# Kernel optimization log

Hardware: AMD Instinct MI355X
Metric: run time of the kernel (lower is better)

Reference implementation:

```python
import jax, jax.numpy as jnp
import numpy as np

B, C, W, H = 4, 512, 64, 64
CK = C // 8  # channels // k


def setup_inputs() -> dict:
    key = jax.random.key(0)
    ks = jax.random.split(key, 10)
    s = 0.02
    return {
        "x": jax.random.normal(ks[0], (B, C, W, H), jnp.float32),
        "wf": jax.random.normal(ks[1], (CK, C), jnp.float32) * s,
        "bf": jax.random.normal(ks[2], (CK,), jnp.float32) * s,
        "wg": jax.random.normal(ks[3], (CK, C), jnp.float32) * s,
        "bg": jax.random.normal(ks[4], (CK,), jnp.float32) * s,
        "wh": jax.random.normal(ks[5], (CK, C), jnp.float32) * s,
        "bh": jax.random.normal(ks[6], (CK,), jnp.float32) * s,
        "wv": jax.random.normal(ks[7], (C, CK), jnp.float32) * s,
        "bv": jax.random.normal(ks[8], (C,), jnp.float32) * s,
        "gamma": jax.random.normal(ks[9], (1,), jnp.float32) * 0.1,
    }


def reference(x, wf, bf, wg, bg, wh, bh, wv, bv, gamma):
    b, c, w, h = x.shape
    n = w * h  # location_num
    xf = x.reshape(b, c, n)  # (B, C, N)
    # conv1x1 projections == per-location matmuls
    f = jnp.einsum('oc,bcn->bon', wf, xf) + bf[None, :, None]  # (B, CK, N)
    g = jnp.einsum('oc,bcn->bon', wg, xf) + bg[None, :, None]
    hh = jnp.einsum('oc,bcn->bon', wh, xf) + bh[None, :, None]
    # beta[b, i, j] = sum_c f[b,c,i] * g[b,c,j]; softmax over dim=1 (i axis)
    beta = jax.nn.softmax(jnp.einsum('bcn,bcm->bnm', f, g), axis=1)  # (B, N, N)
    h2 = jnp.einsum('bcn,bnm->bcm', hh, beta)  # (B, CK, N)
    o = jnp.einsum('oc,bcn->bon', wv, h2) + bv[None, :, None]  # (B, C, N)
    y = gamma[0] * o + xf
    return y.reshape(b, c, w, h)
```

## Files before the change

### kernel.cpp

```cpp
#include <hip/hip_runtime.h>
#include <stdint.h>

#define B_ 4
#define C_ 512
#define N_ 4096
#define D_ 64
#define LOG2E 1.4426950408889634f

typedef __attribute__((ext_vector_type(8))) short short8;
typedef __attribute__((ext_vector_type(4))) float f32x4;
typedef __attribute__((ext_vector_type(16))) float f32x16;
typedef unsigned short ushort_t;

static __device__ __forceinline__ ushort_t f2bf(float f) {
    union { float f; uint32_t u; } v; v.f = f;
    uint32_t u = v.u;
    uint32_t r = u + 0x7FFFu + ((u >> 16) & 1u);
    return (ushort_t)(r >> 16);
}
static __device__ __forceinline__ float bf2f(uint32_t u) {
    union { uint32_t u; float f; } v; v.u = u << 16;
    return v.f;
}
static __device__ __forceinline__ uint32_t cvtpk_bf16(float lo, float hi) {
    uint32_t r;
    asm("v_cvt_pk_bf16_f32 %0, %1, %2" : "=v"(r) : "v"(lo), "v"(hi));
    return r;
}
static __device__ __forceinline__ void gl16(const ushort_t* g, ushort_t* l) {
    __builtin_amdgcn_global_load_lds(
        (const __attribute__((address_space(1))) void*)g,
        (__attribute__((address_space(3))) void*)l, 16, 0, 0);
}

__global__ __launch_bounds__(512) void proj_fgh(
    const float* __restrict__ x,
    const float* __restrict__ wf, const float* __restrict__ bf,
    const float* __restrict__ wg, const float* __restrict__ bg,
    const float* __restrict__ wh, const float* __restrict__ bh,
    ushort_t* __restrict__ Ftf, ushort_t* __restrict__ Gt,
    ushort_t* __restrict__ Vtf)
{
    const int b    = blockIdx.y;
    const int tile = blockIdx.x;
    const int n0   = tile * 64;
    const int tid  = threadIdx.x;
    const int wv   = tid >> 6;
    const int mw   = wv & 3;
    const int hi   = wv >> 2;
    const int lane = tid & 63;
    const int g    = lane >> 4;
    const int r    = lane & 15;

    __shared__ ushort_t As[64][40];
    __shared__ ushort_t Bs[192][40];

    f32x4 acc[6];
    #pragma unroll
    for (int t = 0; t < 6; ++t) acc[t] = (f32x4){0.f, 0.f, 0.f, 0.f};

    const int ka = tid >> 4;
    const int mb = (tid & 15) * 4;
    const int kb = (tid & 7) * 4;
    const int ow = tid >> 3;

    const float* xp  = x  + ((size_t)b * C_ + ka) * N_ + n0 + mb;
    const float* wp0 = wf + (size_t)ow * C_ + kb;
    const float* wp1 = wg + (size_t)ow * C_ + kb;
    const float* wp2 = wh + (size_t)ow * C_ + kb;

    float4 xa = *(const float4*)xp;
    float4 w0 = *(const float4*)wp0;
    float4 w1 = *(const float4*)wp1;
    float4 w2 = *(const float4*)wp2;

    for (int k0 = 0; k0 < C_; k0 += 32) {
        As[mb + 0][ka] = f2bf(xa.x);
        As[mb + 1][ka] = f2bf(xa.y);
        As[mb + 2][ka] = f2bf(xa.z);
        As[mb + 3][ka] = f2bf(xa.w);
        {
            uint2 p0, p1, p2;
            p0.x = cvtpk_bf16(w0.x, w0.y); p0.y = cvtpk_bf16(w0.z, w0.w);
            p1.x = cvtpk_bf16(w1.x, w1.y); p1.y = cvtpk_bf16(w1.z, w1.w);
            p2.x = cvtpk_bf16(w2.x, w2.y); p2.y = cvtpk_bf16(w2.z, w2.w);
            *(uint2*)&Bs[ow][kb]       = p0;
            *(uint2*)&Bs[64 + ow][kb]  = p1;
            *(uint2*)&Bs[128 + ow][kb] = p2;
        }
        if (k0 + 32 < C_) {
            xa = *(const float4*)(xp + (size_t)(k0 + 32) * N_);
            w0 = *(const float4*)(wp0 + k0 + 32);
            w1 = *(const float4*)(wp1 + k0 + 32);
            w2 = *(const float4*)(wp2 + k0 + 32);
        }
        __syncthreads();
        short8 a = *(const short8*)&As[16 * mw + r][8 * g];
        __builtin_amdgcn_s_setprio(1);
        #pragma unroll
        for (int tt = 0; tt < 6; ++tt) {
            const int T = hi * 6 + tt;
            short8 bbv = *(const short8*)&Bs[T * 16 + r][8 * g];
            acc[tt] = __builtin_amdgcn_mfma_f32_16x16x32_bf16(a, bbv, acc[tt], 0, 0, 0);
        }
        __builtin_amdgcn_s_setprio(0);
        __syncthreads();
    }

    #pragma unroll
    for (int u = 0; u < 2; ++u) {
        const int tt = hi ? u : (4 + u);
        const int og = hi ? (32 + u * 16 + r) : (u * 16 + r);
        const float bvv = bg[og];
        #pragma unroll
        for (int j = 0; j < 4; ++j) {
            const int loc = n0 + 16 * mw + 4 * g + j;
            Gt[((size_t)b * N_ + loc) * D_ + og] = f2bf(acc[tt][j] + bvv);
        }
    }

    ushort_t (*bb)[72] = (ushort_t(*)[72])Bs;

    if (hi == 0) {
        #pragma unroll
        for (int tt = 0; tt < 4; ++tt) {
            const int o = tt * 16 + r;
            const float bvv = bf[o];
            #pragma unroll
            for (int j = 0; j < 4; ++j)
                bb[16 * mw + 4 * g + j][o] = f2bf((acc[tt][j] + bvv) * LOG2E);
        }
    }
    __syncthreads();
    {
        const int f  = wv;
        const int cc = f >> 2, s = f & 3;
        short8 v = *(const short8*)&bb[32 * cc + (lane & 31)][16 * s + 8 * (lane >> 5)];
        *(short8*)&Ftf[(((size_t)b * 64 + tile) * 8 + f) * 512 + lane * 8] = v;
    }
    __syncthreads();

    if (hi == 1) {
        #pragma unroll
        for (int tt = 2; tt < 6; ++tt) {
            const int o = (tt - 2) * 16 + r;
            const float bvv = bh[o];
            #pragma unroll
            for (int j = 0; j < 4; ++j)
                bb[16 * mw + 4 * g + j][o] = f2bf(acc[tt][j] + bvv);
        }
    }
    __syncthreads();
    {
        const int f   = wv;
        const int cc  = f >> 2, sub = (f >> 1) & 1, dt = f & 1;
        const int h2l = lane >> 5;
        short8 v;
        #pragma unroll
        for (int e = 0; e < 8; ++e) {
            const int i = 32 * cc + 16 * sub + (e & 3) + 8 * (e >> 2) + 4 * h2l;
            v[e] = (short)bb[i][32 * dt + (lane & 31)];
        }
        *(short8*)&Vtf[(((size_t)b * 64 + tile) * 8 + f) * 512 + lane * 8] = v;
    }
}

__global__ __launch_bounds__(256, 4) void attn(
    const ushort_t* __restrict__ Ftf, const ushort_t* __restrict__ Gt,
    const ushort_t* __restrict__ Vtf,
    ushort_t* __restrict__ Op, float* __restrict__ ml, int ksplit)
{
    const int b    = blockIdx.z;
    const int part = blockIdx.y;
    const int tid  = threadIdx.x;
    const int lane = tid & 63;
    const int wave = tid >> 6;
    const int l31  = lane & 31;
    const int h2   = lane >> 5;
    const int j0   = blockIdx.x * 128 + wave * 32;
    const int NT   = (N_ / ksplit) / 64;
    const int kt0  = part * NT;

    __shared__ __align__(16) ushort_t Ks[2][4096];
    __shared__ __align__(16) ushort_t Vs[2][4096];

    const ushort_t* qrow = Gt + ((size_t)b * N_ + j0 + l31) * D_ + 8 * h2;
    const short8 qf0 = *(const short8*)(qrow);
    const short8 qf1 = *(const short8*)(qrow + 16);
    const short8 qf2 = *(const short8*)(qrow + 32);
    const short8 qf3 = *(const short8*)(qrow + 48);

    const ushort_t* Kt = Ftf + ((size_t)b * 64 + kt0) * 4096;
    const ushort_t* Vt = Vtf + ((size_t)b * 64 + kt0) * 4096;

    f32x16 oA, oB;
    #pragma unroll
    for (int q = 0; q < 16; ++q) { oA[q] = 0.f; oB[q] = 0.f; }
    float l_run = 0.f;

    gl16(Kt + tid * 8,         &Ks[0][tid * 8]);
    gl16(Kt + (tid + 256) * 8, &Ks[0][(tid + 256) * 8]);
    gl16(Vt + tid * 8,         &Vs[0][tid * 8]);
    gl16(Vt + (tid + 256) * 8, &Vs[0][(tid + 256) * 8]);

    int buf = 0;
    for (int t = 0; t < NT; ++t) {
        __syncthreads();
        if (t + 1 < NT) {
            const ushort_t* kg = Kt + (size_t)(t + 1) * 4096;
            const ushort_t* vg = Vt + (size_t)(t + 1) * 4096;
            const int nb = buf ^ 1;
            gl16(kg + tid * 8,         &Ks[nb][tid * 8]);
            gl16(kg + (tid + 256) * 8, &Ks[nb][(tid + 256) * 8]);
            gl16(vg + tid * 8,         &Vs[nb][tid * 8]);
            gl16(vg + (tid + 256) * 8, &Vs[nb][(tid + 256) * 8]);
        }
        #pragma unroll
        for (int cc = 0; cc < 2; ++cc) {
            const ushort_t* kb0 = &Ks[buf][cc * 2048];
            f32x16 sx;
            #pragma unroll
            for (int q = 0; q < 16; ++q) sx[q] = 0.f;
            __builtin_amdgcn_s_setprio(1);
            {
                const short8 k0 = *(const short8*)(kb0 + 0 * 512 + lane * 8);
                sx = __builtin_amdgcn_mfma_f32_32x32x16_bf16(k0, qf0, sx, 0, 0, 0);
                const short8 k1 = *(const short8*)(kb0 + 1 * 512 + lane * 8);
                sx = __builtin_amdgcn_mfma_f32_32x32x16_bf16(k1, qf1, sx, 0, 0, 0);
                const short8 k2 = *(const short8*)(kb0 + 2 * 512 + lane * 8);
                sx = __builtin_amdgcn_mfma_f32_32x32x16_bf16(k2, qf2, sx, 0, 0, 0);
                const short8 k3 = *(const short8*)(kb0 + 3 * 512 + lane * 8);
                sx = __builtin_amdgcn_mfma_f32_32x32x16_bf16(k3, qf3, sx, 0, 0, 0);
            }
            __builtin_amdgcn_s_setprio(0);

            uint32_t pw[8];
            float cs = 0.f;
            #pragma unroll
            for (int q = 0; q < 8; ++q) {
                const float pa = __builtin_amdgcn_exp2f(sx[2 * q]);
                const float pb = __builtin_amdgcn_exp2f(sx[2 * q + 1]);
                cs += pa + pb;
                pw[q] = cvtpk_bf16(pa, pb);
            }
            l_run += cs;

            union { uint32_t w[4]; short8 v; } p0u, p1u;
            p0u.w[0] = pw[0]; p0u.w[1] = pw[1]; p0u.w[2] = pw[2]; p0u.w[3] = pw[3];
            p1u.w[0] = pw[4]; p1u.w[1] = pw[5]; p1u.w[2] = pw[6]; p1u.w[3] = pw[7];

            const ushort_t* vb0 = &Vs[buf][cc * 2048];
            __builtin_amdgcn_s_setprio(1);
            {
                const short8 v00 = *(const short8*)(vb0 + 0 * 512 + lane * 8);
                oA = __builtin_amdgcn_mfma_f32_32x32x16_bf16(v00, p0u.v, oA, 0, 0, 0);
                const short8 v01 = *(const short8*)(vb0 + 1 * 512 + lane * 8);
                oB = __builtin_amdgcn_mfma_f32_32x32x16_bf16(v01, p0u.v, oB, 0, 0, 0);
                const short8 v10 = *(const short8*)(vb0 + 2 * 512 + lane * 8);
                oA = __builtin_amdgcn_mfma_f32_32x32x16_bf16(v10, p1u.v, oA, 0, 0, 0);
                const short8 v11 = *(const short8*)(vb0 + 3 * 512 + lane * 8);
                oB = __builtin_amdgcn_mfma_f32_32x32x16_bf16(v11, p1u.v, oB, 0, 0, 0);
            }
            __builtin_amdgcn_s_setprio(0);
        }
        buf ^= 1;
    }

    const float lt = l_run + __shfl_xor(l_run, 32);

    ushort_t* orow = Op + (((size_t)b * ksplit + part) * N_ + j0 + l31) * D_;
    #pragma unroll
    for (int q = 0; q < 4; ++q) {
        const int d0 = 8 * q + 4 * h2;
        uint2 ua, ub;
        ua.x = cvtpk_bf16(oA[4 * q],     oA[4 * q + 1]);
        ua.y = cvtpk_bf16(oA[4 * q + 2], oA[4 * q + 3]);
        *(uint2*)&orow[d0] = ua;
        ub.x = cvtpk_bf16(oB[4 * q],     oB[4 * q + 1]);
        ub.y = cvtpk_bf16(oB[4 * q + 2], oB[4 * q + 3]);
        *(uint2*)&orow[32 + d0] = ub;
    }
    if (h2 == 0)
        ml[((size_t)b * ksplit + part) * N_ + j0 + l31] = lt;
}

__global__ __launch_bounds__(512) void reduce_outproj(
    const ushort_t* __restrict__ Op, const float* __restrict__ ml,
    const float* __restrict__ wv, const float* __restrict__ bv,
    const float* __restrict__ gamma, const float* __restrict__ x,
    float* __restrict__ y, int ksplit)
{
    const int b    = blockIdx.y;
    const int n0   = blockIdx.x * 64;
    const int tid  = threadIdx.x;
    const int wv8  = tid >> 6;
    const int lane = tid & 63;
    const int g    = lane >> 4;
    const int r    = lane & 15;

    __shared__ ushort_t Os[64][72];

    {
        const int loc = tid >> 3;
        const int k8  = (tid & 7) * 8;
        float L = 0.f;
        float v[8] = {0.f, 0.f, 0.f, 0.f, 0.f, 0.f, 0.f, 0.f};
        for (int p = 0; p < ksplit; ++p) {
            const size_t base = ((size_t)b * ksplit + p) * N_ + n0 + loc;
            L += ml[base];
            uint4 u = *(const uint4*)&Op[base * D_ + k8];
            v[0] += bf2f(u.x & 0xffffu); v[1] += bf2f(u.x >> 16);
            v[2] += bf2f(u.y & 0xffffu); v[3] += bf2f(u.y >> 16);
            v[4] += bf2f(u.z & 0xffffu); v[5] += bf2f(u.z >> 16);
            v[6] += bf2f(u.w & 0xffffu); v[7] += bf2f(u.w >> 16);
        }
        const float inv = 1.0f / L;
        uint4 o;
        o.x = cvtpk_bf16(v[0] * inv, v[1] * inv);
        o.y = cvtpk_bf16(v[2] * inv, v[3] * inv);
        o.z = cvtpk_bf16(v[4] * inv, v[5] * inv);
        o.w = cvtpk_bf16(v[6] * inv, v[7] * inv);
        *(uint4*)&Os[loc][k8] = o;
    }
    __syncthreads();

    short8 a[4][2];
    #pragma unroll
    for (int cs = 0; cs < 4; ++cs) {
        const float* wrow = wv + (size_t)(wv8 * 64 + cs * 16 + r) * D_ + 8 * g;
        const float4 wa = *(const float4*)(wrow);
        const float4 wb = *(const float4*)(wrow + 4);
        const float4 wc = *(const float4*)(wrow + 32);
        const float4 wd = *(const float4*)(wrow + 36);
        uint32_t* a0 = (uint32_t*)&a[cs][0];
        uint32_t* a1 = (uint32_t*)&a[cs][1];
        a0[0] = cvtpk_bf16(wa.x, wa.y); a0[1] = cvtpk_bf16(wa.z, wa.w);
        a0[2] = cvtpk_bf16(wb.x, wb.y); a0[3] = cvtpk_bf16(wb.z, wb.w);
        a1[0] = cvtpk_bf16(wc.x, wc.y); a1[1] = cvtpk_bf16(wc.z, wc.w);
        a1[2] = cvtpk_bf16(wd.x, wd.y); a1[3] = cvtpk_bf16(wd.z, wd.w);
    }

    f32x4 acc[4][4];
    #pragma unroll
    for (int cs = 0; cs < 4; ++cs)
        #pragma unroll
        for (int t = 0; t < 4; ++t) acc[cs][t] = (f32x4){0.f, 0.f, 0.f, 0.f};

    #pragma unroll
    for (int t = 0; t < 4; ++t) {
        const short8 b0 = *(const short8*)&Os[16 * t + r][8 * g];
        const short8 b1 = *(const short8*)&Os[16 * t + r][32 + 8 * g];
        __builtin_amdgcn_s_setprio(1);
        #pragma unroll
        for (int cs = 0; cs < 4; ++cs) {
            acc[cs][t] = __builtin_amdgcn_mfma_f32_16x16x32_bf16(a[cs][0], b0, acc[cs][t], 0, 0, 0);
            acc[cs][t] = __builtin_amdgcn_mfma_f32_16x16x32_bf16(a[cs][1], b1, acc[cs][t], 0, 0, 0);
        }
        __builtin_amdgcn_s_setprio(0);
    }

    const float gm = *gamma;
    #pragma unroll
    for (int cs = 0; cs < 4; ++cs) {
        #pragma unroll
        for (int t = 0; t < 4; ++t) {
            #pragma unroll
            for (int j = 0; j < 4; ++j) {
                const int co = wv8 * 64 + cs * 16 + 4 * g + j;
                const int n  = n0 + 16 * t + r;
                const size_t idx = ((size_t)b * C_ + co) * N_ + n;
                y[idx] = gm * (acc[cs][t][j] + bv[co]) + x[idx];
            }
        }
    }
}

extern "C" void kernel_launch(void* const* d_in, const int* in_sizes, int n_in,
                              void* d_out, int out_size, void* d_ws, size_t ws_size,
                              hipStream_t stream) {
    const float* x     = (const float*)d_in[0];
    const float* wf    = (const float*)d_in[1];
    const float* bf    = (const float*)d_in[2];
    const float* wg    = (const float*)d_in[3];
    const float* bg    = (const float*)d_in[4];
    const float* wh    = (const float*)d_in[5];
    const float* bh    = (const float*)d_in[6];
    const float* wv    = (const float*)d_in[7];
    const float* bv    = (const float*)d_in[8];
    const float* gamma = (const float*)d_in[9];
    float* y = (float*)d_out;

    const size_t plane = (size_t)B_ * N_ * D_;
    ushort_t* Ftf = (ushort_t*)d_ws;
    ushort_t* Gt  = Ftf + plane;
    ushort_t* Vtf = Gt + plane;
    ushort_t* Op  = Vtf + plane;

    int KS = 8;
    while (KS > 1) {
        const size_t need = 3 * plane * 2 + (size_t)KS * plane * 2
                          + (size_t)B_ * KS * N_ * sizeof(float);
        if (need <= ws_size) break;
        KS >>= 1;
    }
    float* ml = (float*)(Op + (size_t)KS * plane);

    proj_fgh<<<dim3(N_ / 64, B_), 512, 0, stream>>>(
        x, wf, bf, wg, bg, wh, bh, Ftf, Gt, Vtf);
    attn<<<dim3(N_ / 128, KS, B_), 256, 0, stream>>>(
        Ftf, Gt, Vtf, Op, ml, KS);
    reduce_outproj<<<dim3(N_ / 64, B_), 512, 0, stream>>>(
        Op, ml, wv, bv, gamma, x, y, KS);
}
```

Measured before the change: 60.11 us.

## Halve projection tile to 32 locations to double block count

The projection kernel now processes 32 spatial locations per block instead of 64, launching twice as many blocks so more CUs are occupied. Each wave computes 3 MFMA tiles (one each for F, G, H) instead of 6, and the epilogue writes F and H into separate shared-memory regions with a single barrier, splitting the Ftf/Vtf stores between the two thread halves. The weight tiles are still loaded and converted per block, so weight traffic and conversion work double relative to the x data.

```diff
diff --git a/kernel.cpp b/kernel.cpp
--- a/kernel.cpp
+++ b/kernel.cpp
@@ -42,34 +42,36 @@
     ushort_t* __restrict__ Vtf)
 {
     const int b    = blockIdx.y;
-    const int tile = blockIdx.x;
-    const int n0   = tile * 64;
+    const int nb   = blockIdx.x;
+    const int tile = nb >> 1;
+    const int cc   = nb & 1;
+    const int n0   = nb * 32;
     const int tid  = threadIdx.x;
     const int wv   = tid >> 6;
-    const int mw   = wv & 3;
-    const int hi   = wv >> 2;
+    const int mw   = wv & 1;
+    const int hi   = wv >> 1;
     const int lane = tid & 63;
     const int g    = lane >> 4;
     const int r    = lane & 15;
 
-    __shared__ ushort_t As[64][40];
+    __shared__ ushort_t As[32][40];
     __shared__ ushort_t Bs[192][40];
 
-    f32x4 acc[6];
-    #pragma unroll
-    for (int t = 0; t < 6; ++t) acc[t] = (f32x4){0.f, 0.f, 0.f, 0.f};
+    f32x4 acc[3];
+    #pragma unroll
+    for (int t = 0; t < 3; ++t) acc[t] = (f32x4){0.f, 0.f, 0.f, 0.f};
 
     const int ka = tid >> 4;
-    const int mb = (tid & 15) * 4;
+    const int mb = (tid & 15) * 2;
+    const int ow = tid >> 3;
     const int kb = (tid & 7) * 4;
-    const int ow = tid >> 3;
 
     const float* xp  = x  + ((size_t)b * C_ + ka) * N_ + n0 + mb;
     const float* wp0 = wf + (size_t)ow * C_ + kb;
     const float* wp1 = wg + (size_t)ow * C_ + kb;
     const float* wp2 = wh + (size_t)ow * C_ + kb;
 
-    float4 xa = *(const float4*)xp;
+    float2 xa = *(const float2*)xp;
     float4 w0 = *(const float4*)wp0;
     float4 w1 = *(const float4*)wp1;
     float4 w2 = *(const float4*)wp2;
@@ -77,8 +79,6 @@
     for (int k0 = 0; k0 < C_; k0 += 32) {
         As[mb + 0][ka] = f2bf(xa.x);
         As[mb + 1][ka] = f2bf(xa.y);
-        As[mb + 2][ka] = f2bf(xa.z);
-        As[mb + 3][ka] = f2bf(xa.w);
         {
             uint2 p0, p1, p2;
             p0.x = cvtpk_bf16(w0.x, w0.y); p0.y = cvtpk_bf16(w0.z, w0.w);
@@ -89,7 +89,7 @@
             *(uint2*)&Bs[128 + ow][kb] = p2;
         }
         if (k0 + 32 < C_) {
-            xa = *(const float4*)(xp + (size_t)(k0 + 32) * N_);
+            xa = *(const float2*)(xp + (size_t)(k0 + 32) * N_);
             w0 = *(const float4*)(wp0 + k0 + 32);
             w1 = *(const float4*)(wp1 + k0 + 32);
             w2 = *(const float4*)(wp2 + k0 + 32);
@@ -98,8 +98,8 @@
         short8 a = *(const short8*)&As[16 * mw + r][8 * g];
         __builtin_amdgcn_s_setprio(1);
         #pragma unroll
-        for (int tt = 0; tt < 6; ++tt) {
-            const int T = hi * 6 + tt;
+        for (int tt = 0; tt < 3; ++tt) {
+            const int T = tt * 4 + hi;
             short8 bbv = *(const short8*)&Bs[T * 16 + r][8 * g];
             acc[tt] = __builtin_amdgcn_mfma_f32_16x16x32_bf16(a, bbv, acc[tt], 0, 0, 0);
         }
@@ -107,61 +107,55 @@
         __syncthreads();
     }
 
-    #pragma unroll
-    for (int u = 0; u < 2; ++u) {
-        const int tt = hi ? u : (4 + u);
-        const int og = hi ? (32 + u * 16 + r) : (u * 16 + r);
+    {
+        const int og = hi * 16 + r;
         const float bvv = bg[og];
         #pragma unroll
         for (int j = 0; j < 4; ++j) {
             const int loc = n0 + 16 * mw + 4 * g + j;
-            Gt[((size_t)b * N_ + loc) * D_ + og] = f2bf(acc[tt][j] + bvv);
-        }
-    }
-
-    ushort_t (*bb)[72] = (ushort_t(*)[72])Bs;
-
-    if (hi == 0) {
-        #pragma unroll
-        for (int tt = 0; tt < 4; ++tt) {
-            const int o = tt * 16 + r;
-            const float bvv = bf[o];
-            #pragma unroll
-            for (int j = 0; j < 4; ++j)
-                bb[16 * mw + 4 * g + j][o] = f2bf((acc[tt][j] + bvv) * LOG2E);
-        }
+            Gt[((size_t)b * N_ + loc) * D_ + og] = f2bf(acc[1][j] + bvv);
+        }
+    }
+
+    ushort_t (*bbF)[72] = (ushort_t(*)[72])&Bs[0][0];
+    ushort_t (*bbH)[72] = (ushort_t(*)[72])(&Bs[0][0] + 32 * 72);
+
+    {
+        const int o = hi * 16 + r;
+        const float bvv = bf[o];
+        #pragma unroll
+        for (int j = 0; j < 4; ++j)
+            bbF[16 * mw + 4 * g + j][o] = f2bf((acc[0][j] + bvv) * LOG2E);
+    }
+    {
+        const int o = hi * 16 + r;
+        const float bvv = bh[o];
+        #pragma unroll
+        for (int j = 0; j < 4; ++j)
+            bbH[16 * mw + 4 * g + j][o] = f2bf(acc[2][j] + bvv);
     }
     __syncthreads();
-    {
-        const int f  = wv;
-        const int cc = f >> 2, s = f & 3;
-        short8 v = *(const short8*)&bb[32 * cc + (lane & 31)][16 * s + 8 * (lane >> 5)];
-        *(short8*)&Ftf[(((size_t)b * 64 + tile) * 8 + f) * 512 + lane * 8] = v;
-    }
-    __syncthreads();
-
-    if (hi == 1) {
-        #pragma unroll
-        for (int tt = 2; tt < 6; ++tt) {
-            const int o = (tt - 2) * 16 + r;
-            const float bvv = bh[o];
-            #pragma unroll
-            for (int j = 0; j < 4; ++j)
-                bb[16 * mw + 4 * g + j][o] = f2bf(acc[tt][j] + bvv);
-        }
-    }
-    __syncthreads();
-    {
-        const int f   = wv;
-        const int cc  = f >> 2, sub = (f >> 1) & 1, dt = f & 1;
-        const int h2l = lane >> 5;
+
+    if (tid < 256) {
+        const int s = (tid >> 6) & 3;
+        const int l = tid & 63;
+        short8 v = *(const short8*)&bbF[l & 31][16 * s + 8 * (l >> 5)];
+        const int f = cc * 4 + s;
+        *(short8*)&Ftf[(((size_t)b * 64 + tile) * 8 + f) * 512 + l * 8] = v;
+    } else {
+        const int u   = tid & 255;
+        const int fi  = u >> 6;
+        const int sub = fi >> 1, dt = fi & 1;
+        const int l   = u & 63;
+        const int h2l = l >> 5;
         short8 v;
         #pragma unroll
         for (int e = 0; e < 8; ++e) {
-            const int i = 32 * cc + 16 * sub + (e & 3) + 8 * (e >> 2) + 4 * h2l;
-            v[e] = (short)bb[i][32 * dt + (lane & 31)];
-        }
-        *(short8*)&Vtf[(((size_t)b * 64 + tile) * 8 + f) * 512 + lane * 8] = v;
+            const int i = 16 * sub + (e & 3) + 8 * (e >> 2) + 4 * h2l;
+            v[e] = (short)bbH[i][32 * dt + (l & 31)];
+        }
+        const int f = cc * 4 + sub * 2 + dt;
+        *(short8*)&Vtf[(((size_t)b * 64 + tile) * 8 + f) * 512 + l * 8] = v;
     }
 }
 
@@ -405,7 +399,7 @@
     }
     float* ml = (float*)(Op + (size_t)KS * plane);
 
-    proj_fgh<<<dim3(N_ / 64, B_), 512, 0, stream>>>(
+    proj_fgh<<<dim3(N_ / 32, B_), 512, 0, stream>>>(
         x, wf, bf, wg, bg, wh, bh, Ftf, Gt, Vtf);
     attn<<<dim3(N_ / 128, KS, B_), 256, 0, stream>>>(
         Ftf, Gt, Vtf, Op, ml, KS);
```

Result: no change. 59.44 us (-1.1%).
